# Kernel optimization log

Measured on AMD Instinct MI355X. Metric: run time of the kernel, lower is better.

The kernel has to match this reference:

```python
import jax, jax.numpy as jnp
import numpy as np

D_MODEL = 1024
D_STATE = 16
D_CONV = 3
EXPAND = 2
MLP_RATIO = 4
HEADDIM = 64
D_INNER = EXPAND * D_MODEL            # 2048
NHEADS = D_INNER // HEADDIM           # 32
CONV_DIM = D_INNER + 2 * D_STATE      # x, B, C all go through the depthwise conv
D_IN_PROJ = 2 * D_INNER + 2 * D_STATE + NHEADS


def rmsnorm(x, w, eps=1e-6):
    return x * jax.lax.rsqrt(jnp.mean(x * x, axis=-1, keepdims=True) + eps) * w


def silu(x):
    return x * jax.nn.sigmoid(x)


def causal_depthwise_conv(x, w, b):
    # x: (B, L, C); w: (C, K); b: (C,)  -- causal depthwise conv over L
    B, L, C = x.shape
    K = w.shape[1]
    xp = jnp.pad(x, ((0, 0), (K - 1, 0), (0, 0)))
    out = b
    for k in range(K):  # tiny fixed loop over kernel taps (K=3)
        out = out + w[:, k] * xp[:, k:k + L, :]
    return out


def mamba2(h, W_in, conv_w, conv_b, dt_bias, A_log, D, norm_gate_w, W_out):
    B, L, _ = h.shape
    zxbcdt = h @ W_in  # (B, L, D_IN_PROJ)
    z = zxbcdt[..., :D_INNER]
    xBC = zxbcdt[..., D_INNER:D_INNER + CONV_DIM]
    dt = jax.nn.softplus(zxbcdt[..., D_INNER + CONV_DIM:] + dt_bias)  # (B, L, H)

    xBC = silu(causal_depthwise_conv(xBC, conv_w, conv_b))
    x = xBC[..., :D_INNER].reshape(B, L, NHEADS, HEADDIM)
    Bmat = xBC[..., D_INNER:D_INNER + D_STATE]   # (B, L, N)
    Cmat = xBC[..., D_INNER + D_STATE:]          # (B, L, N)

    A = -jnp.exp(A_log)                          # (H,)
    dA = jnp.exp(dt * A)                         # (B, L, H)
    dBx = jnp.einsum('blhp,bln,blh->blhpn', x, Bmat, dt)  # (B, L, H, P, N)

    def step(state, inp):
        dA_t, dBx_t = inp                        # (B,H), (B,H,P,N)
        state = state * dA_t[:, :, None, None] + dBx_t
        return state, state

    s0 = jnp.zeros((B, NHEADS, HEADDIM, D_STATE), dtype=h.dtype)
    _, states = jax.lax.scan(step, s0,
                             (jnp.moveaxis(dA, 1, 0), jnp.moveaxis(dBx, 1, 0)))
    # states: (L, B, H, P, N)
    y = jnp.einsum('lbhpn,bln->blhp', states, Cmat)
    y = y + D[None, None, :, None] * x
    y = y.reshape(B, L, D_INNER)
    y = rmsnorm(y * silu(z), norm_gate_w, eps=1e-5)  # gated RMSNorm as in Mamba2
    return y @ W_out


def setup_inputs() -> dict:
    key = jax.random.key(0)
    ks = jax.random.split(key, 12)
    f = jnp.float32
    d = {}
    d['x'] = jax.random.normal(ks[0], (2, 2048, D_MODEL), dtype=f)
    d['norm1_w'] = jnp.ones((D_MODEL,), f)
    d['W_in'] = jax.random.normal(ks[1], (D_MODEL, D_IN_PROJ), f) * (D_MODEL ** -0.5)
    d['conv_w'] = jax.random.normal(ks[2], (CONV_DIM, D_CONV), f) * 0.2
    d['conv_b'] = jnp.zeros((CONV_DIM,), f)
    d['dt_bias'] = jnp.log(jnp.expm1(jax.random.uniform(ks[3], (NHEADS,), f, 0.001, 0.1)))
    d['A_log'] = jnp.log(jax.random.uniform(ks[4], (NHEADS,), f, 1.0, 16.0))
    d['D'] = jnp.ones((NHEADS,), f)
    d['norm_gate_w'] = jnp.ones((D_INNER,), f)
    d['W_out'] = jax.random.normal(ks[5], (D_INNER, D_MODEL), f) * (D_INNER ** -0.5)
    d['norm2_w'] = jnp.ones((D_MODEL,), f)
    d['mlp_w1'] = jax.random.normal(ks[6], (D_MODEL, D_MODEL * MLP_RATIO), f) * (D_MODEL ** -0.5)
    d['mlp_b1'] = jnp.zeros((D_MODEL * MLP_RATIO,), f)
    d['mlp_w2'] = jax.random.normal(ks[7], (D_MODEL * MLP_RATIO, D_MODEL), f) * ((D_MODEL * MLP_RATIO) ** -0.5)
    d['mlp_b2'] = jnp.zeros((D_MODEL,), f)
    return d


def reference(x, norm1_w, W_in, conv_w, conv_b, dt_bias, A_log, D,
              norm_gate_w, W_out, norm2_w, mlp_w1, mlp_b1, mlp_w2, mlp_b2):
    h = rmsnorm(x, norm1_w)
    h = mamba2(h, W_in, conv_w, conv_b, dt_bias, A_log, D, norm_gate_w, W_out)
    x = x + h
    h = rmsnorm(x, norm2_w)
    h = silu(h @ mlp_w1 + mlp_b1) @ mlp_w2 + mlp_b2
    return x + h
```

## Files before the change

### kernel.cpp

```cpp
#include <hip/hip_runtime.h>

typedef __bf16 bf16;
typedef __bf16 bf16x4 __attribute__((ext_vector_type(4)));
typedef __bf16 bf16x8 __attribute__((ext_vector_type(8)));
typedef float  f32x4  __attribute__((ext_vector_type(4)));

#define BATCH  2
#define SEQ    2048
#define ROWS   (BATCH*SEQ)
#define DMODEL 1024
#define DINNER 2048
#define DSTATE 16
#define NH     32
#define HD     64
#define CONVD  2080
#define DPROJ  4160
#define DMLP   4096
#define DTOFF  (DINNER + CONVD)
#define CS     64
#define NCHUNK (SEQ/CS)
#define NSPLIT 2

__device__ __forceinline__ float sigmoidf_(float x) { return 1.f / (1.f + expf(-x)); }

__device__ __forceinline__ float blockSum256(float v) {
    #pragma unroll
    for (int o = 32; o > 0; o >>= 1) v += __shfl_down(v, o);
    __shared__ float sb[4];
    const int tid = threadIdx.x;
    if ((tid & 63) == 0) sb[tid >> 6] = v;
    __syncthreads();
    return sb[0] + sb[1] + sb[2] + sb[3];
}

__device__ __forceinline__ void gload_lds16(const bf16* g, bf16* l) {
    __builtin_amdgcn_global_load_lds((const __attribute__((address_space(1))) void*)g,
                                     (__attribute__((address_space(3))) void*)l, 16, 0, 0);
}

__device__ __forceinline__ int xcd_swz(int orig, int nwg) {
    const int q = nwg >> 3, r = nwg & 7;
    const int x = orig & 7, i = orig >> 3;
    return (x < r ? x * (q + 1) : r * (q + 1) + (x - r) * q) + i;
}

#define TSEG0 4160
#define TSEG1 (TSEG0 + 2048)
#define TSEG2 (TSEG1 + 4096)
#define TSEG3 (TSEG2 + 4096)
__global__ __launch_bounds__(256) void transpose_all_k(
    const float* __restrict__ s0, bf16* __restrict__ d0,
    const float* __restrict__ s1, bf16* __restrict__ d1,
    const float* __restrict__ s2, bf16* __restrict__ d2,
    const float* __restrict__ s3, bf16* __restrict__ d3)
{
    const int gb = blockIdx.x;
    const float* in; bf16* out; int L, tC, R, C;
    if (gb < TSEG0)      { in = s0; out = d0; L = gb;         tC = 130; R = 1024; C = 4160; }
    else if (gb < TSEG1) { in = s1; out = d1; L = gb - TSEG0; tC = 32;  R = 2048; C = 1024; }
    else if (gb < TSEG2) { in = s2; out = d2; L = gb - TSEG1; tC = 128; R = 1024; C = 4096; }
    else                 { in = s3; out = d3; L = gb - TSEG2; tC = 32;  R = 4096; C = 1024; }
    const int bx = (L % tC) * 32, by = (L / tC) * 32;
    __shared__ float t[32][33];
    const int tx = threadIdx.x, ty = threadIdx.y;
    #pragma unroll
    for (int i = 0; i < 4; ++i)
        t[ty + i * 8][tx] = in[(size_t)(by + ty + i * 8) * C + bx + tx];
    __syncthreads();
    #pragma unroll
    for (int i = 0; i < 4; ++i)
        out[(size_t)(bx + ty + i * 8) * R + by + tx] = (bf16)t[tx][ty + i * 8];
}

template<int EPI>
__global__ __launch_bounds__(512) void gemm_bt(
    const bf16* __restrict__ A, const bf16* __restrict__ BT,
    int M, int N, int K, int nbx, int nby,
    bf16* __restrict__ outb, float* __restrict__ outf,
    const float* __restrict__ bias, float* __restrict__ dtout, size_t pstride)
{
    __shared__ __align__(16) bf16 SH[4][128 * 64];
    const int nwg = (int)gridDim.x;
    const int wg  = xcd_swz((int)blockIdx.x, nwg);
    const int bx  = wg % nbx;
    const int t2  = wg / nbx;
    const int by  = t2 % nby;
    const int sl  = t2 / nby;
    const int ns  = nwg / (nbx * nby);
    const int Ks  = K / ns;
    const int kbeg = sl * Ks;

    const int tid  = threadIdx.x;
    const int brow = by * 128;
    const int bcol = bx * 128;
    const int lane = tid & 63;
    const int wid  = tid >> 6;
    const int wm = wid >> 1, wn = wid & 1;
    const int lr = lane & 15, lk = lane >> 4;
    const int X  = lr & 7;
    const int off0 = ((lk) ^ X) * 8;
    const int off1 = ((4 + lk) ^ X) * 8;

    f32x4 acc[2][4] = {};

    size_t aoff[2], boff[2];
    #pragma unroll
    for (int i = 0; i < 2; ++i) {
        const int g = tid + i * 512;
        const int srow = g >> 3;
        const int scol = ((g & 7) ^ (srow & 7)) * 8;
        aoff[i] = (size_t)(brow + srow) * K + scol;
        int bn = bcol + srow; if (bn > N - 1) bn = N - 1;
        boff[i] = (size_t)bn * K + scol;
    }

    auto stage = [&](int buf, int k0) {
        #pragma unroll
        for (int i = 0; i < 2; ++i) {
            gload_lds16(A + aoff[i] + k0, SH[buf] + (tid + i * 512) * 8);
            gload_lds16(BT + boff[i] + k0, SH[2 + buf] + (tid + i * 512) * 8);
        }
    };

    const int nt = Ks >> 6;
    stage(0, kbeg);
    __syncthreads();
    for (int t = 0; t < nt; ++t) {
        const int cur = t & 1;
        if (t + 1 < nt) stage(cur ^ 1, kbeg + (t + 1) * 64);
        #pragma unroll
        for (int kk = 0; kk < 2; ++kk) {
            const int off = kk ? off1 : off0;
            bf16x8 af[2], bfr[4];
            #pragma unroll
            for (int m = 0; m < 2; ++m)
                af[m] = *(const bf16x8*)(SH[cur] + (wm * 32 + m * 16 + lr) * 64 + off);
            #pragma unroll
            for (int n = 0; n < 4; ++n)
                bfr[n] = *(const bf16x8*)(SH[2 + cur] + (wn * 64 + n * 16 + lr) * 64 + off);
            #pragma unroll
            for (int m = 0; m < 2; ++m)
                #pragma unroll
                for (int n = 0; n < 4; ++n)
                    acc[m][n] = __builtin_amdgcn_mfma_f32_16x16x32_bf16(af[m], bfr[n], acc[m][n], 0, 0, 0);
        }
        __syncthreads();
    }

    if constexpr (EPI == 0) {
        if (bcol + 128 > DTOFF) {
            #pragma unroll
            for (int m = 0; m < 2; ++m) {
                const int grow = brow + wm * 32 + m * 16 + lk * 4;
                #pragma unroll
                for (int n = 0; n < 4; ++n) {
                    const int gcol = bcol + wn * 64 + n * 16 + lr;
                    if (gcol < DTOFF || gcol >= N) continue;
                    #pragma unroll
                    for (int j = 0; j < 4; ++j)
                        dtout[(size_t)(grow + j) * NH + (gcol - DTOFF)] = acc[m][n][j];
                }
            }
        }
    }

    bf16* Cs = &SH[0][0];
    #pragma unroll
    for (int m = 0; m < 2; ++m) {
        const int r0 = wm * 32 + m * 16 + lk * 4;
        #pragma unroll
        for (int n = 0; n < 4; ++n) {
            const int c = wn * 64 + n * 16 + lr;
            #pragma unroll
            for (int j = 0; j < 4; ++j) {
                float v = acc[m][n][j];
                if constexpr (EPI == 1) {
                    v += bias[bcol + c];
                    v = v * sigmoidf_(v);
                }
                Cs[(r0 + j) * 132 + c] = (bf16)v;
            }
        }
    }
    __syncthreads();
    #pragma unroll
    for (int i = 0; i < 4; ++i) {
        const int chunk = tid + i * 512;
        const int r = chunk >> 4;
        const int c = (chunk & 15) * 8;
        const int gcol = bcol + c;
        if (gcol >= N) continue;
        const bf16x8 val = *(const bf16x8*)(Cs + r * 132 + c);
        const size_t idx = (size_t)(brow + r) * N + gcol;
        if constexpr (EPI == 2) *(bf16x8*)(outb + pstride * sl + idx) = val;
        else                    *(bf16x8*)(outb + idx) = val;
    }
}

__global__ __launch_bounds__(256) void reduce_norm_k(const bf16* __restrict__ part,
                                                     const float* __restrict__ res,
                                                     const float* __restrict__ w,
                                                     float* __restrict__ x2,
                                                     bf16* __restrict__ h2) {
    const int row = blockIdx.x, tid = threadIdx.x;
    const size_t MN = (size_t)ROWS * DMODEL;
    const size_t i = (size_t)row * DMODEL + tid * 4;
    const bf16x4 a = *(const bf16x4*)(part + i);
    const bf16x4 b = *(const bf16x4*)(part + MN + i);
    const float4 r = *(const float4*)(res + i);
    const float ra[4] = { r.x, r.y, r.z, r.w };
    float f[4];
    #pragma unroll
    for (int j = 0; j < 4; ++j) f[j] = (float)a[j] + (float)b[j] + ra[j];
    *(float4*)(x2 + i) = make_float4(f[0], f[1], f[2], f[3]);
    float ss = f[0]*f[0] + f[1]*f[1] + f[2]*f[2] + f[3]*f[3];
    ss = blockSum256(ss);
    const float scale = rsqrtf(ss * (1.f / DMODEL) + 1e-6f);
    const float4 wv = *(const float4*)(w + tid * 4);
    const float wa[4] = { wv.x, wv.y, wv.z, wv.w };
    bf16x4 o;
    #pragma unroll
    for (int j = 0; j < 4; ++j) o[j] = (bf16)(f[j] * scale * wa[j]);
    *(bf16x4*)(h2 + i) = o;
}

__global__ __launch_bounds__(256) void reduce_k(const bf16* __restrict__ part,
                                                const float* __restrict__ res,
                                                const float* __restrict__ bias,
                                                float* __restrict__ out, int MN) {
    const int i = (blockIdx.x * 256 + threadIdx.x) * 4;
    if (i >= MN) return;
    const bf16x4 a = *(const bf16x4*)(part + i);
    const bf16x4 b = *(const bf16x4*)(part + (size_t)MN + i);
    const float4 r = *(const float4*)(res + i);
    const float ra[4] = { r.x, r.y, r.z, r.w };
    const int col = i & (DMODEL - 1);
    float o[4];
    #pragma unroll
    for (int j = 0; j < 4; ++j) o[j] = (float)a[j] + (float)b[j] + ra[j] + bias[col + j];
    *(float4*)(out + i) = make_float4(o[0], o[1], o[2], o[3]);
}

__global__ __launch_bounds__(256) void rmsnorm_k(const float* __restrict__ in,
                                                 const float* __restrict__ w,
                                                 bf16* __restrict__ out, float eps) {
    const int row = blockIdx.x, tid = threadIdx.x;
    const float4 v = *(const float4*)(in + (size_t)row * DMODEL + tid * 4);
    float f[4] = { v.x, v.y, v.z, v.w };
    float ss = f[0]*f[0] + f[1]*f[1] + f[2]*f[2] + f[3]*f[3];
    ss = blockSum256(ss);
    const float scale = rsqrtf(ss * (1.f / DMODEL) + eps);
    const float4 wv = *(const float4*)(w + tid * 4);
    const float wa[4] = { wv.x, wv.y, wv.z, wv.w };
    bf16x4 o;
    #pragma unroll
    for (int j = 0; j < 4; ++j) o[j] = (bf16)(f[j] * scale * wa[j]);
    *(bf16x4*)(out + (size_t)row * DMODEL + tid * 4) = o;
}

__global__ __launch_bounds__(256) void rmsgate_k(const bf16* __restrict__ y,
                                                 const bf16* __restrict__ zx,
                                                 const float* __restrict__ w,
                                                 bf16* __restrict__ out) {
    const int row = blockIdx.x, tid = threadIdx.x;
    const bf16* yr = y + (size_t)row * DINNER;
    const bf16* zr = zx + (size_t)row * DPROJ;
    float vals[8];
    float ss = 0.f;
    #pragma unroll
    for (int i = 0; i < 2; ++i) {
        const bf16x4 yv = *(const bf16x4*)(yr + tid * 8 + i * 4);
        const bf16x4 zv = *(const bf16x4*)(zr + tid * 8 + i * 4);
        #pragma unroll
        for (int j = 0; j < 4; ++j) {
            const float z = (float)zv[j];
            const float t = (float)yv[j] * (z * sigmoidf_(z));
            vals[i * 4 + j] = t;
            ss += t * t;
        }
    }
    ss = blockSum256(ss);
    const float scale = rsqrtf(ss * (1.f / DINNER) + 1e-5f);
    bf16* orow = out + (size_t)row * DINNER + tid * 8;
    #pragma unroll
    for (int i = 0; i < 2; ++i) {
        bf16x4 o;
        #pragma unroll
        for (int j = 0; j < 4; ++j)
            o[j] = (bf16)(vals[i * 4 + j] * scale * w[tid * 8 + i * 4 + j]);
        *(bf16x4*)(orow + i * 4) = o;
    }
}

__global__ __launch_bounds__(256) void conv_silu_k(const bf16* __restrict__ zx,
                                                   const float* __restrict__ cw,
                                                   const float* __restrict__ cb,
                                                   bf16* __restrict__ xBC) {
    const int idx = blockIdx.x * 256 + threadIdx.x;
    if (idx >= ROWS * CONVD) return;
    const int c  = idx % CONVD;
    const int bl = idx / CONVD;
    const int l  = bl % SEQ;
    float acc = cb[c];
    const bf16* col = zx + (size_t)bl * DPROJ + DINNER + c;
    if (l >= 2) acc += cw[c * 3 + 0] * (float)col[-2 * DPROJ];
    if (l >= 1) acc += cw[c * 3 + 1] * (float)col[-1 * DPROJ];
    acc += cw[c * 3 + 2] * (float)col[0];
    acc = acc * sigmoidf_(acc);
    xBC[(size_t)bl * CONVD + c] = (bf16)acc;
}

__global__ __launch_bounds__(256) void dtda_k(const float* __restrict__ dtraw,
                                              const float* __restrict__ dt_bias,
                                              const float* __restrict__ A_log,
                                              float* __restrict__ dtb,
                                              float* __restrict__ dab) {
    const int idx = blockIdx.x * 256 + threadIdx.x;
    if (idx >= ROWS * NH) return;
    const int h = idx & (NH - 1);
    const float raw = dtraw[idx] + dt_bias[h];
    const float dt = raw > 20.f ? raw : log1pf(expf(raw));
    const float dA = expf(-expf(A_log[h]) * dt);
    dtb[idx] = dt;
    dab[idx] = dA;
}

__global__ __launch_bounds__(256) void scan1_k(const bf16* __restrict__ xBC,
                                               const float* __restrict__ dtb,
                                               const float* __restrict__ dab,
                                               float* __restrict__ Sloc,
                                               float* __restrict__ Pc) {
    const int c = blockIdx.x & (NCHUNK - 1);
    const int h = (blockIdx.x >> 5) & (NH - 1);
    const int b = blockIdx.x >> 10;
    const int tid = threadIdx.x;
    const int p  = tid >> 2;
    const int nq = (tid & 3) * 4;
    const size_t rb = (size_t)b * SEQ + c * CS;
    const bf16* xrow = xBC + rb * CONVD + h * HD + p;
    const bf16* Brow = xBC + rb * CONVD + DINNER + nq;
    const float* dtp = dtb + rb * NH + h;
    const float* dap = dab + rb * NH + h;
    float s0 = 0.f, s1 = 0.f, s2 = 0.f, s3 = 0.f, P = 1.f;
    for (int l = 0; l < CS; ++l) {
        const float xv  = (float)xrow[(size_t)l * CONVD];
        const bf16x4 Bv = *(const bf16x4*)(Brow + (size_t)l * CONVD);
        const float dtv = dtp[l * NH];
        const float dav = dap[l * NH];
        const float xdt = xv * dtv;
        s0 = s0 * dav + xdt * (float)Bv[0];
        s1 = s1 * dav + xdt * (float)Bv[1];
        s2 = s2 * dav + xdt * (float)Bv[2];
        s3 = s3 * dav + xdt * (float)Bv[3];
        P *= dav;
    }
    float4* dst = (float4*)(Sloc + (size_t)blockIdx.x * 1024 + tid * 4);
    *dst = make_float4(s0, s1, s2, s3);
    if (tid == 0) Pc[blockIdx.x] = P;
}

__global__ __launch_bounds__(256) void scan2_k(const float* __restrict__ Sloc,
                                               const float* __restrict__ Pc,
                                               float* __restrict__ Sini) {
    const int bh = blockIdx.x;
    const int tid = threadIdx.x;
    const size_t base = (size_t)bh * NCHUNK;
    float c0 = 0.f, c1 = 0.f, c2 = 0.f, c3 = 0.f;
    for (int c = 0; c < NCHUNK; ++c) {
        *(float4*)(Sini + (base + c) * 1024 + tid * 4) = make_float4(c0, c1, c2, c3);
        const float4 sl = *(const float4*)(Sloc + (base + c) * 1024 + tid * 4);
        const float P = Pc[base + c];
        c0 = c0 * P + sl.x;
        c1 = c1 * P + sl.y;
        c2 = c2 * P + sl.z;
        c3 = c3 * P + sl.w;
    }
}

__global__ __launch_bounds__(256) void scan3_k(const bf16* __restrict__ xBC,
                                               const float* __restrict__ dtb,
                                               const float* __restrict__ dab,
                                               const float* __restrict__ Dp,
                                               const float* __restrict__ Sini,
                                               bf16* __restrict__ y) {
    const int c = blockIdx.x & (NCHUNK - 1);
    const int h = (blockIdx.x >> 5) & (NH - 1);
    const int b = blockIdx.x >> 10;
    const int tid = threadIdx.x;
    const int p  = tid >> 2;
    const int nq = (tid & 3) * 4;
    const float Dh = Dp[h];
    const size_t rb = (size_t)b * SEQ + c * CS;
    const bf16* xrow = xBC + rb * CONVD + h * HD + p;
    const bf16* Brow = xBC + rb * CONVD + DINNER + nq;
    const bf16* Crow = xBC + rb * CONVD + DINNER + DSTATE + nq;
    const float* dtp = dtb + rb * NH + h;
    const float* dap = dab + rb * NH + h;
    bf16* yp = y + rb * DINNER + h * HD + p;
    const float4 si = *(const float4*)(Sini + (size_t)blockIdx.x * 1024 + tid * 4);
    float s0 = si.x, s1 = si.y, s2 = si.z, s3 = si.w;
    for (int l = 0; l < CS; ++l) {
        const float xv  = (float)xrow[(size_t)l * CONVD];
        const bf16x4 Bv = *(const bf16x4*)(Brow + (size_t)l * CONVD);
        const bf16x4 Cv = *(const bf16x4*)(Crow + (size_t)l * CONVD);
        const float dtv = dtp[l * NH];
        const float dav = dap[l * NH];
        const float xdt = xv * dtv;
        s0 = s0 * dav + xdt * (float)Bv[0];
        s1 = s1 * dav + xdt * (float)Bv[1];
        s2 = s2 * dav + xdt * (float)Bv[2];
        s3 = s3 * dav + xdt * (float)Bv[3];
        float part = s0 * (float)Cv[0] + s1 * (float)Cv[1] + s2 * (float)Cv[2] + s3 * (float)Cv[3];
        part += __shfl_xor(part, 1);
        part += __shfl_xor(part, 2);
        if ((tid & 3) == 0) yp[(size_t)l * DINNER] = (bf16)(part + Dh * xv);
    }
}

extern "C" void kernel_launch(void* const* d_in, const int* in_sizes, int n_in,
                              void* d_out, int out_size, void* d_ws, size_t ws_size,
                              hipStream_t stream) {
    const float* x       = (const float*)d_in[0];
    const float* n1w     = (const float*)d_in[1];
    const float* W_in    = (const float*)d_in[2];
    const float* conv_w  = (const float*)d_in[3];
    const float* conv_b  = (const float*)d_in[4];
    const float* dt_bias = (const float*)d_in[5];
    const float* A_log   = (const float*)d_in[6];
    const float* Dp      = (const float*)d_in[7];
    const float* ngw     = (const float*)d_in[8];
    const float* W_out   = (const float*)d_in[9];
    const float* n2w     = (const float*)d_in[10];
    const float* w1      = (const float*)d_in[11];
    const float* b1      = (const float*)d_in[12];
    const float* w2      = (const float*)d_in[13];
    const float* b2      = (const float*)d_in[14];
    float* out = (float*)d_out;

    char* p = (char*)d_ws;
    auto alloc = [&](size_t bytes) -> char* {
        char* q = p;
        p += (bytes + 255) & ~(size_t)255;
        return q;
    };
    bf16*  W_inT  = (bf16*) alloc((size_t)DPROJ  * DMODEL * 2);
    bf16*  W_outT = (bf16*) alloc((size_t)DMODEL * DINNER * 2);
    bf16*  w1T    = (bf16*) alloc((size_t)DMLP   * DMODEL * 2);
    bf16*  w2T    = (bf16*) alloc((size_t)DMODEL * DMLP   * 2);
    bf16*  h1     = (bf16*) alloc((size_t)ROWS * DMODEL * 2);
    bf16*  zx     = (bf16*) alloc((size_t)ROWS * DPROJ  * 2);
    float* dtraw  = (float*)alloc((size_t)ROWS * NH * 4);
    bf16*  xBC    = (bf16*) alloc((size_t)ROWS * CONVD * 2);
    float* dtb    = (float*)alloc((size_t)ROWS * NH * 4);
    float* dab    = (float*)alloc((size_t)ROWS * NH * 4);
    bf16*  ybuf   = (bf16*) alloc((size_t)ROWS * DINNER * 2);
    bf16*  ynorm  = (bf16*) alloc((size_t)ROWS * DINNER * 2);
    float* x2     = (float*)alloc((size_t)ROWS * DMODEL * 4);
    bf16*  h2     = (bf16*) alloc((size_t)ROWS * DMODEL * 2);
    bf16*  mid    = (bf16*) alloc((size_t)ROWS * DMLP * 2);
    float* Sloc   = (float*)alloc((size_t)BATCH * NH * NCHUNK * 1024 * 4);
    float* Sini   = (float*)alloc((size_t)BATCH * NH * NCHUNK * 1024 * 4);
    float* Pc     = (float*)alloc((size_t)BATCH * NH * NCHUNK * 4);
    bf16*  part   = zx;
    const size_t pstride = (size_t)ROWS * DMODEL;
    (void)ws_size; (void)in_sizes; (void)n_in; (void)out_size;

    transpose_all_k<<<TSEG3, dim3(32, 8), 0, stream>>>(
        W_in, W_inT, W_out, W_outT, w1, w1T, w2, w2T);

    rmsnorm_k<<<ROWS, 256, 0, stream>>>(x, n1w, h1, 1e-6f);

    gemm_bt<0><<<33 * 32, 512, 0, stream>>>(
        h1, W_inT, ROWS, DPROJ, DMODEL, 33, 32, zx, nullptr, nullptr, dtraw, 0);

    conv_silu_k<<<(ROWS * CONVD + 255) / 256, 256, 0, stream>>>(zx, conv_w, conv_b, xBC);
    dtda_k<<<(ROWS * NH + 255) / 256, 256, 0, stream>>>(dtraw, dt_bias, A_log, dtb, dab);

    scan1_k<<<BATCH * NH * NCHUNK, 256, 0, stream>>>(xBC, dtb, dab, Sloc, Pc);
    scan2_k<<<BATCH * NH, 256, 0, stream>>>(Sloc, Pc, Sini);
    scan3_k<<<BATCH * NH * NCHUNK, 256, 0, stream>>>(xBC, dtb, dab, Dp, Sini, ybuf);

    rmsgate_k<<<ROWS, 256, 0, stream>>>(ybuf, zx, ngw, ynorm);

    gemm_bt<2><<<8 * 32 * NSPLIT, 512, 0, stream>>>(
        ynorm, W_outT, ROWS, DMODEL, DINNER, 8, 32, part, nullptr, nullptr, nullptr, pstride);
    reduce_norm_k<<<ROWS, 256, 0, stream>>>(part, x, n2w, x2, h2);

    gemm_bt<1><<<32 * 32, 512, 0, stream>>>(
        h2, w1T, ROWS, DMLP, DMODEL, 32, 32, mid, nullptr, b1, nullptr, 0);

    gemm_bt<2><<<8 * 32 * NSPLIT, 512, 0, stream>>>(
        mid, w2T, ROWS, DMODEL, DMLP, 8, 32, part, nullptr, nullptr, nullptr, pstride);
    reduce_k<<<(ROWS * DMODEL / 4 + 255) / 256, 256, 0, stream>>>(
        part, x2, b2, out, ROWS * DMODEL);
}
```

Before: 310.6 us.

## Single-buffer GEMM LDS, swizzle epilogue tile, split-K by four

The GEMM drops LDS double buffering and keeps one A/B tile, halving shared memory so more workgroups can be resident per CU. The epilogue staging tile moves from padded rows of 132 to a 128-wide XOR-swizzled layout that fits in the smaller buffer. Split-K rises from 2 to 4, and both reduction kernels now sum four partial slices. In exchange, global loads no longer overlap MFMA work inside a workgroup, and the partial-sum buffers and reduction traffic double.

New measurement: 326.1 us. 1.05x slower.

```diff
diff --git a/kernel.cpp b/kernel.cpp
--- a/kernel.cpp
+++ b/kernel.cpp
@@ -19,7 +19,7 @@
 #define DTOFF  (DINNER + CONVD)
 #define CS     64
 #define NCHUNK (SEQ/CS)
-#define NSPLIT 2
+#define NSPLIT 4
 
 __device__ __forceinline__ float sigmoidf_(float x) { return 1.f / (1.f + expf(-x)); }
 
@@ -79,7 +79,7 @@
     bf16* __restrict__ outb, float* __restrict__ outf,
     const float* __restrict__ bias, float* __restrict__ dtout, size_t pstride)
 {
-    __shared__ __align__(16) bf16 SH[4][128 * 64];
+    __shared__ __align__(16) bf16 SH[2][128 * 64];
     const int nwg = (int)gridDim.x;
     const int wg  = xcd_swz((int)blockIdx.x, nwg);
     const int bx  = wg % nbx;
@@ -114,30 +114,25 @@
         boff[i] = (size_t)bn * K + scol;
     }
 
-    auto stage = [&](int buf, int k0) {
+    const int nt = Ks >> 6;
+    for (int t = 0; t < nt; ++t) {
+        const int k0 = kbeg + t * 64;
         #pragma unroll
         for (int i = 0; i < 2; ++i) {
-            gload_lds16(A + aoff[i] + k0, SH[buf] + (tid + i * 512) * 8);
-            gload_lds16(BT + boff[i] + k0, SH[2 + buf] + (tid + i * 512) * 8);
+            gload_lds16(A + aoff[i] + k0, SH[0] + (tid + i * 512) * 8);
+            gload_lds16(BT + boff[i] + k0, SH[1] + (tid + i * 512) * 8);
         }
-    };
-
-    const int nt = Ks >> 6;
-    stage(0, kbeg);
-    __syncthreads();
-    for (int t = 0; t < nt; ++t) {
-        const int cur = t & 1;
-        if (t + 1 < nt) stage(cur ^ 1, kbeg + (t + 1) * 64);
+        __syncthreads();
         #pragma unroll
         for (int kk = 0; kk < 2; ++kk) {
             const int off = kk ? off1 : off0;
             bf16x8 af[2], bfr[4];
             #pragma unroll
             for (int m = 0; m < 2; ++m)
-                af[m] = *(const bf16x8*)(SH[cur] + (wm * 32 + m * 16 + lr) * 64 + off);
+                af[m] = *(const bf16x8*)(SH[0] + (wm * 32 + m * 16 + lr) * 64 + off);
             #pragma unroll
             for (int n = 0; n < 4; ++n)
-                bfr[n] = *(const bf16x8*)(SH[2 + cur] + (wn * 64 + n * 16 + lr) * 64 + off);
+                bfr[n] = *(const bf16x8*)(SH[1] + (wn * 64 + n * 16 + lr) * 64 + off);
             #pragma unroll
             for (int m = 0; m < 2; ++m)
                 #pragma unroll
@@ -178,7 +173,8 @@
                     v += bias[bcol + c];
                     v = v * sigmoidf_(v);
                 }
-                Cs[(r0 + j) * 132 + c] = (bf16)v;
+                const int r = r0 + j;
+                Cs[r * 128 + (((c >> 3) ^ (r & 7)) << 3) + (c & 7)] = (bf16)v;
             }
         }
     }
@@ -187,10 +183,10 @@
     for (int i = 0; i < 4; ++i) {
         const int chunk = tid + i * 512;
         const int r = chunk >> 4;
-        const int c = (chunk & 15) * 8;
-        const int gcol = bcol + c;
+        const int g = chunk & 15;
+        const int gcol = bcol + g * 8;
         if (gcol >= N) continue;
-        const bf16x8 val = *(const bf16x8*)(Cs + r * 132 + c);
+        const bf16x8 val = *(const bf16x8*)(Cs + r * 128 + ((g ^ (r & 7)) << 3));
         const size_t idx = (size_t)(brow + r) * N + gcol;
         if constexpr (EPI == 2) *(bf16x8*)(outb + pstride * sl + idx) = val;
         else                    *(bf16x8*)(outb + idx) = val;
@@ -207,11 +203,14 @@
     const size_t i = (size_t)row * DMODEL + tid * 4;
     const bf16x4 a = *(const bf16x4*)(part + i);
     const bf16x4 b = *(const bf16x4*)(part + MN + i);
+    const bf16x4 c = *(const bf16x4*)(part + 2 * MN + i);
+    const bf16x4 d = *(const bf16x4*)(part + 3 * MN + i);
     const float4 r = *(const float4*)(res + i);
     const float ra[4] = { r.x, r.y, r.z, r.w };
     float f[4];
     #pragma unroll
-    for (int j = 0; j < 4; ++j) f[j] = (float)a[j] + (float)b[j] + ra[j];
+    for (int j = 0; j < 4; ++j)
+        f[j] = ((float)a[j] + (float)b[j]) + ((float)c[j] + (float)d[j]) + ra[j];
     *(float4*)(x2 + i) = make_float4(f[0], f[1], f[2], f[3]);
     float ss = f[0]*f[0] + f[1]*f[1] + f[2]*f[2] + f[3]*f[3];
     ss = blockSum256(ss);
@@ -232,12 +231,15 @@
     if (i >= MN) return;
     const bf16x4 a = *(const bf16x4*)(part + i);
     const bf16x4 b = *(const bf16x4*)(part + (size_t)MN + i);
+    const bf16x4 c = *(const bf16x4*)(part + 2 * (size_t)MN + i);
+    const bf16x4 d = *(const bf16x4*)(part + 3 * (size_t)MN + i);
     const float4 r = *(const float4*)(res + i);
     const float ra[4] = { r.x, r.y, r.z, r.w };
     const int col = i & (DMODEL - 1);
     float o[4];
     #pragma unroll
-    for (int j = 0; j < 4; ++j) o[j] = (float)a[j] + (float)b[j] + ra[j] + bias[col + j];
+    for (int j = 0; j < 4; ++j)
+        o[j] = ((float)a[j] + (float)b[j]) + ((float)c[j] + (float)d[j]) + ra[j] + bias[col + j];
     *(float4*)(out + i) = make_float4(o[0], o[1], o[2], o[3]);
 }
 
```
